# Kernel optimization log

Measured on AMD Instinct MI355X. Metric: run time of the kernel, lower is better.

Reference implementation:

```python
import jax, jax.numpy as jnp
import numpy as np

NUM_TOKENS = 16384
COMPACT = 8192
HIDDEN = 2048
INTER = 8192


def setup_inputs() -> dict:
    key = jax.random.key(0)
    k_x, k_fg, k_sc, k_wg, k_wu, k_wd = jax.random.split(key, 6)
    x = jax.random.normal(k_x, (NUM_TOKENS, HIDDEN), dtype=jnp.float32)
    fold_gather = jax.random.randint(k_fg, (COMPACT,), 0, NUM_TOKENS, dtype=jnp.int32)
    scatter_indices = jax.random.randint(k_sc, (NUM_TOKENS,), 0, COMPACT, dtype=jnp.int32)
    # torch nn.Linear weights are [out_features, in_features]
    s_h = 1.0 / np.sqrt(HIDDEN)
    s_i = 1.0 / np.sqrt(INTER)
    W_gate = jax.random.uniform(k_wg, (INTER, HIDDEN), jnp.float32, -s_h, s_h)
    W_up = jax.random.uniform(k_wu, (INTER, HIDDEN), jnp.float32, -s_h, s_h)
    W_down = jax.random.uniform(k_wd, (HIDDEN, INTER), jnp.float32, -s_i, s_i)
    return {"x": x, "W_gate": W_gate, "W_up": W_up, "W_down": W_down,
            "fold_gather": fold_gather, "scatter_indices": scatter_indices}


def reference(x, W_gate, W_up, W_down, fold_gather, scatter_indices):
    # gather original tokens into compact space
    x_compact = jnp.take(x, fold_gather, axis=0)               # [C, H]
    gate = jax.nn.silu(jnp.einsum('ch,ih->ci', x_compact, W_gate))  # [C, I]
    up = jnp.einsum('ch,ih->ci', x_compact, W_up)               # [C, I]
    down = jnp.einsum('ci,hi->ch', gate * up, W_down)           # [C, H]
    # scatter compact results back to every original token slot
    return jnp.take(down, scatter_indices, axis=0)              # [N, H]
```

## Files before the change

kernel.cpp:

```cpp
#include <hip/hip_runtime.h>
#include <hip/hip_bf16.h>
#include <stdint.h>

#define HIDDEN  2048
#define INTER   8192
#define COMPACT 8192
#define NTOK    16384

#define NT_GU (HIDDEN / 64)
#define NT_DN (INTER / 64)

typedef unsigned short ushort_t;
typedef float  f32x4  __attribute__((ext_vector_type(4)));
typedef __bf16 bf16x8 __attribute__((ext_vector_type(8)));

#define VMCNT(n) asm volatile("s_waitcnt vmcnt(" #n ")" ::: "memory")
#define FENCE()  asm volatile("" ::: "memory")
#define BARRIER() do { FENCE(); __builtin_amdgcn_s_barrier(); FENCE(); } while (0)

__device__ __align__(16) ushort_t g_xc[(size_t)COMPACT * HIDDEN];
__device__ __align__(16) ushort_t g_wg[(size_t)INTER * HIDDEN];
__device__ __align__(16) ushort_t g_wu[(size_t)INTER * HIDDEN];
__device__ __align__(16) ushort_t g_wd[(size_t)HIDDEN * INTER];
__device__ __align__(16) float    g_dn[(size_t)COMPACT * HIDDEN];

__device__ __forceinline__ ushort_t f2bf(float f) {
    uint32_t u = __builtin_bit_cast(uint32_t, f);
    uint32_t lsb = (u >> 16) & 1u;
    u += 0x7fffu + lsb;
    return (ushort_t)(u >> 16);
}

__device__ __forceinline__ void async_cp16(const void* g, void* l) {
    __builtin_amdgcn_global_load_lds(
        (__attribute__((address_space(1))) void*)((void*)g),
        (__attribute__((address_space(3))) void*)l,
        16, 0, 0);
}

__device__ __forceinline__ bf16x8 ldfrag(const ushort_t* m, int row, int slot) {
    return *(const bf16x8*)(m + row * 64 + slot * 8);
}

__global__ __launch_bounds__(256)
void k_gather_cast(const float* __restrict__ x, const int* __restrict__ fg)
{
    const int c = blockIdx.x;
    const int t = threadIdx.x;
    const float4* src = (const float4*)(x + (size_t)fg[c] * HIDDEN) + (t << 1);
    float4 a = src[0], b = src[1];
    union { ushort_t u[8]; uint4 v; } p;
    p.u[0] = f2bf(a.x); p.u[1] = f2bf(a.y); p.u[2] = f2bf(a.z); p.u[3] = f2bf(a.w);
    p.u[4] = f2bf(b.x); p.u[5] = f2bf(b.y); p.u[6] = f2bf(b.z); p.u[7] = f2bf(b.w);
    *((uint4*)(g_xc + (size_t)c * HIDDEN) + t) = p.v;
}

template<int W>
__global__ __launch_bounds__(256)
void k_cast(const float* __restrict__ src)
{
    ushort_t* __restrict__ dst = (W == 0) ? g_wg : (W == 1) ? g_wu : g_wd;
    const size_t g = (size_t)blockIdx.x * 256 + threadIdx.x;
    const float4* s = (const float4*)src + (g << 1);
    float4 a = s[0], b = s[1];
    union { ushort_t u[8]; uint4 v; } p;
    p.u[0] = f2bf(a.x); p.u[1] = f2bf(a.y); p.u[2] = f2bf(a.z); p.u[3] = f2bf(a.w);
    p.u[4] = f2bf(b.x); p.u[5] = f2bf(b.y); p.u[6] = f2bf(b.z); p.u[7] = f2bf(b.w);
    *((uint4*)dst + g) = p.v;
}

#define MFMA16(ACC, AF, BF)                                                    \
    _Pragma("unroll")                                                          \
    for (int i = 0; i < 4; ++i)                                                \
        _Pragma("unroll")                                                      \
        for (int j = 0; j < 2; ++j) {                                          \
            ACC[i][j] = __builtin_amdgcn_mfma_f32_16x16x32_bf16(AF[i][0], BF[j][0], ACC[i][j], 0, 0, 0); \
            ACC[i][j] = __builtin_amdgcn_mfma_f32_16x16x32_bf16(AF[i][1], BF[j][1], ACC[i][j], 0, 0, 0); \
        }

__global__ __launch_bounds__(512, 2)
void k_gateup(ushort_t* __restrict__ h)
{
    __shared__ __align__(16) ushort_t As[2][256 * 64];
    __shared__ __align__(16) ushort_t Gs[2][128 * 64];
    __shared__ __align__(16) ushort_t Us[2][128 * 64];

    const int tid  = threadIdx.x;
    const int lane = tid & 63;
    const int wv   = tid >> 6;
    const int wr   = wv >> 2;
    const int wc   = wv & 3;
    const int lr   = lane & 15;
    const int q    = lane >> 4;
    const int sl0  = q ^ (lr & 7);
    const int sl1  = sl0 ^ 4;
    const int srow = tid >> 3;
    const int scol = ((lane & 7) ^ (lane >> 3)) << 3;
    const int lofs = tid * 8;

    const int bm0 = blockIdx.y << 8;
    const int bn0 = blockIdx.x << 7;

    const ushort_t* pA = g_xc + (size_t)(bm0 + srow) * HIDDEN + scol;
    const ushort_t* pG = g_wg + (size_t)(bn0 + srow) * HIDDEN + scol;
    const ushort_t* pU = g_wu + (size_t)(bn0 + srow) * HIDDEN + scol;
    const size_t rS = (size_t)64 * HIDDEN;

    f32x4 ag0[4][2], ag1[4][2], au0[4][2], au1[4][2];
    #pragma unroll
    for (int i = 0; i < 4; ++i)
        #pragma unroll
        for (int j = 0; j < 2; ++j) {
            ag0[i][j] = (f32x4){0.f,0.f,0.f,0.f};
            ag1[i][j] = (f32x4){0.f,0.f,0.f,0.f};
            au0[i][j] = (f32x4){0.f,0.f,0.f,0.f};
            au1[i][j] = (f32x4){0.f,0.f,0.f,0.f};
        }

    {
        ushort_t* An = As[0]; ushort_t* Gn = Gs[0]; ushort_t* Un = Us[0];
        async_cp16(pA,          An + lofs);
        async_cp16(pA + rS,     An + 4096 + lofs);
        async_cp16(pG,          Gn + lofs);
        async_cp16(pG + rS,     Gn + 4096 + lofs);
        async_cp16(pU,          Un + lofs);
        async_cp16(pU + rS,     Un + 4096 + lofs);
        async_cp16(pA + 2*rS,   An + 8192 + lofs);
        async_cp16(pA + 3*rS,   An + 12288 + lofs);
        pA += 64; pG += 64; pU += 64;
        VMCNT(0);
        BARRIER();
    }

    for (int t = 0; t < NT_GU; ++t) {
        const ushort_t* Ac = As[t & 1];
        const ushort_t* Gc = Gs[t & 1];
        const ushort_t* Uc = Us[t & 1];
        ushort_t* An = As[(t & 1) ^ 1];
        ushort_t* Gn = Gs[(t & 1) ^ 1];
        ushort_t* Un = Us[(t & 1) ^ 1];
        const bool more = (t + 1 < NT_GU);

        bf16x8 af[4][2], bg[2][2], bu[2][2];

        #pragma unroll
        for (int i = 0; i < 4; ++i) {
            const int row = wr * 64 + i * 16 + lr;
            af[i][0] = ldfrag(Ac, row, sl0);
            af[i][1] = ldfrag(Ac, row, sl1);
        }
        #pragma unroll
        for (int j = 0; j < 2; ++j) {
            const int row = wc * 32 + j * 16 + lr;
            bg[j][0] = ldfrag(Gc, row, sl0);
            bg[j][1] = ldfrag(Gc, row, sl1);
        }
        if (more) {
            async_cp16(pA,      An + lofs);
            async_cp16(pA + rS, An + 4096 + lofs);
            VMCNT(4);
        } else {
            VMCNT(2);
        }
        BARRIER();
        __builtin_amdgcn_s_setprio(1);
        MFMA16(ag0, af, bg);
        __builtin_amdgcn_s_setprio(0);
        BARRIER();

        #pragma unroll
        for (int j = 0; j < 2; ++j) {
            const int row = wc * 32 + j * 16 + lr;
            bu[j][0] = ldfrag(Uc, row, sl0);
            bu[j][1] = ldfrag(Uc, row, sl1);
        }
        if (more) {
            async_cp16(pG,      Gn + lofs);
            async_cp16(pG + rS, Gn + 4096 + lofs);
            VMCNT(4);
        } else {
            VMCNT(0);
        }
        BARRIER();
        __builtin_amdgcn_s_setprio(1);
        MFMA16(au0, af, bu);
        __builtin_amdgcn_s_setprio(0);
        BARRIER();

        #pragma unroll
        for (int i = 0; i < 4; ++i) {
            const int row = 128 + wr * 64 + i * 16 + lr;
            af[i][0] = ldfrag(Ac, row, sl0);
            af[i][1] = ldfrag(Ac, row, sl1);
        }
        if (more) {
            async_cp16(pU,      Un + lofs);
            async_cp16(pU + rS, Un + 4096 + lofs);
        }
        BARRIER();
        __builtin_amdgcn_s_setprio(1);
        MFMA16(ag1, af, bg);
        __builtin_amdgcn_s_setprio(0);
        BARRIER();

        if (more) {
            async_cp16(pA + 2*rS, An + 8192 + lofs);
            async_cp16(pA + 3*rS, An + 12288 + lofs);
        }
        VMCNT(4);
        BARRIER();
        __builtin_amdgcn_s_setprio(1);
        MFMA16(au1, af, bu);
        __builtin_amdgcn_s_setprio(0);
        BARRIER();

        pA += 64; pG += 64; pU += 64;
    }

    const int or0 = bm0 + wr * 64 + (q << 2);
    const int oc  = bn0 + wc * 32 + lr;
    #define GU_STORE(AG, AU, MH)                                               \
        _Pragma("unroll")                                                      \
        for (int i = 0; i < 4; ++i)                                            \
            _Pragma("unroll")                                                  \
            for (int j = 0; j < 2; ++j)                                        \
                _Pragma("unroll")                                              \
                for (int r = 0; r < 4; ++r) {                                  \
                    float g = AG[i][j][r];                                     \
                    float u = AU[i][j][r];                                     \
                    float s = g / (1.0f + __expf(-g));                         \
                    h[(size_t)(or0 + (MH)*128 + i*16 + r) * INTER + (oc + j*16)] = f2bf(s * u); \
                }
    GU_STORE(ag0, au0, 0)
    GU_STORE(ag1, au1, 1)
    #undef GU_STORE
}

__global__ __launch_bounds__(512, 2)
void k_down(const ushort_t* __restrict__ hbuf)
{
    __shared__ __align__(16) ushort_t As[2][256 * 64];
    __shared__ __align__(16) ushort_t Bs[2][256 * 64];

    const int tid  = threadIdx.x;
    const int lane = tid & 63;
    const int wv   = tid >> 6;
    const int wr   = wv >> 2;
    const int wc   = wv & 3;
    const int lr   = lane & 15;
    const int q    = lane >> 4;
    const int sl0  = q ^ (lr & 7);
    const int sl1  = sl0 ^ 4;
    const int srow = tid >> 3;
    const int scol = ((lane & 7) ^ (lane >> 3)) << 3;
    const int lofs = tid * 8;

    const int bm0 = blockIdx.y << 8;
    const int bn0 = blockIdx.x << 8;

    const ushort_t* pH = hbuf + (size_t)(bm0 + srow) * INTER + scol;
    const ushort_t* pW = g_wd + (size_t)(bn0 + srow) * INTER + scol;
    const size_t rS = (size_t)64 * INTER;

    f32x4 c00[4][2], c01[4][2], c10[4][2], c11[4][2];
    #pragma unroll
    for (int i = 0; i < 4; ++i)
        #pragma unroll
        for (int j = 0; j < 2; ++j) {
            c00[i][j] = (f32x4){0.f,0.f,0.f,0.f};
            c01[i][j] = (f32x4){0.f,0.f,0.f,0.f};
            c10[i][j] = (f32x4){0.f,0.f,0.f,0.f};
            c11[i][j] = (f32x4){0.f,0.f,0.f,0.f};
        }

    {
        ushort_t* An = As[0]; ushort_t* Bn = Bs[0];
        async_cp16(pH,          An + lofs);
        async_cp16(pH + rS,     An + 4096 + lofs);
        async_cp16(pW,          Bn + lofs);
        async_cp16(pW + rS,     Bn + 4096 + lofs);
        async_cp16(pW + 2*rS,   Bn + 8192 + lofs);
        async_cp16(pW + 3*rS,   Bn + 12288 + lofs);
        async_cp16(pH + 2*rS,   An + 8192 + lofs);
        async_cp16(pH + 3*rS,   An + 12288 + lofs);
        pH += 64; pW += 64;
        VMCNT(0);
        BARRIER();
    }

    for (int t = 0; t < NT_DN; ++t) {
        const ushort_t* Ac = As[t & 1];
        const ushort_t* Bc = Bs[t & 1];
        ushort_t* An = As[(t & 1) ^ 1];
        ushort_t* Bn = Bs[(t & 1) ^ 1];
        const bool more = (t + 1 < NT_DN);

        bf16x8 af[4][2], b0[2][2], b1[2][2];

        #pragma unroll
        for (int i = 0; i < 4; ++i) {
            const int row = wr * 64 + i * 16 + lr;
            af[i][0] = ldfrag(Ac, row, sl0);
            af[i][1] = ldfrag(Ac, row, sl1);
        }
        #pragma unroll
        for (int j = 0; j < 2; ++j) {
            const int row = wc * 32 + j * 16 + lr;
            b0[j][0] = ldfrag(Bc, row, sl0);
            b0[j][1] = ldfrag(Bc, row, sl1);
        }
        if (more) {
            async_cp16(pH,      An + lofs);
            async_cp16(pH + rS, An + 4096 + lofs);
            VMCNT(4);
        } else {
            VMCNT(2);
        }
        BARRIER();
        __builtin_amdgcn_s_setprio(1);
        MFMA16(c00, af, b0);
        __builtin_amdgcn_s_setprio(0);
        BARRIER();

        #pragma unroll
        for (int j = 0; j < 2; ++j) {
            const int row = 128 + wc * 32 + j * 16 + lr;
            b1[j][0] = ldfrag(Bc, row, sl0);
            b1[j][1] = ldfrag(Bc, row, sl1);
        }
        if (more) {
            async_cp16(pW,      Bn + lofs);
            async_cp16(pW + rS, Bn + 4096 + lofs);
            VMCNT(4);
        } else {
            VMCNT(0);
        }
        BARRIER();
        __builtin_amdgcn_s_setprio(1);
        MFMA16(c01, af, b1);
        __builtin_amdgcn_s_setprio(0);
        BARRIER();

        #pragma unroll
        for (int i = 0; i < 4; ++i) {
            const int row = 128 + wr * 64 + i * 16 + lr;
            af[i][0] = ldfrag(Ac, row, sl0);
            af[i][1] = ldfrag(Ac, row, sl1);
        }
        if (more) {
            async_cp16(pW + 2*rS, Bn + 8192 + lofs);
            async_cp16(pW + 3*rS, Bn + 12288 + lofs);
        }
        BARRIER();
        __builtin_amdgcn_s_setprio(1);
        MFMA16(c10, af, b0);
        __builtin_amdgcn_s_setprio(0);
        BARRIER();

        if (more) {
            async_cp16(pH + 2*rS, An + 8192 + lofs);
            async_cp16(pH + 3*rS, An + 12288 + lofs);
        }
        VMCNT(4);
        BARRIER();
        __builtin_amdgcn_s_setprio(1);
        MFMA16(c11, af, b1);
        __builtin_amdgcn_s_setprio(0);
        BARRIER();

        pH += 64; pW += 64;
    }

    const int or0 = bm0 + wr * 64 + (q << 2);
    const int oc  = bn0 + wc * 32 + lr;
    #define DN_STORE(CC, MH, NH)                                               \
        _Pragma("unroll")                                                      \
        for (int i = 0; i < 4; ++i)                                            \
            _Pragma("unroll")                                                  \
            for (int j = 0; j < 2; ++j)                                        \
                _Pragma("unroll")                                              \
                for (int r = 0; r < 4; ++r)                                    \
                    g_dn[(size_t)(or0 + (MH)*128 + i*16 + r) * HIDDEN + (oc + (NH)*128 + j*16)] = CC[i][j][r];
    DN_STORE(c00, 0, 0)
    DN_STORE(c01, 0, 1)
    DN_STORE(c10, 1, 0)
    DN_STORE(c11, 1, 1)
    #undef DN_STORE
}

__global__ __launch_bounds__(256)
void k_scatter(const int* __restrict__ sc,
               float4* __restrict__ out)
{
    const int gid = blockIdx.x * 256 + threadIdx.x;
    const int row = gid >> 9;
    const int ch  = gid & 511;
    const int s = sc[row];
    out[((size_t)row << 9) + ch] = ((const float4*)g_dn)[((size_t)s << 9) + ch];
}

extern "C" void kernel_launch(void* const* d_in, const int* in_sizes, int n_in,
                              void* d_out, int out_size, void* d_ws, size_t ws_size,
                              hipStream_t stream)
{
    (void)in_sizes; (void)n_in; (void)out_size; (void)d_ws; (void)ws_size;

    const float* x  = (const float*)d_in[0];
    const float* Wg = (const float*)d_in[1];
    const float* Wu = (const float*)d_in[2];
    const float* Wd = (const float*)d_in[3];
    const int* fg = (const int*)d_in[4];
    const int* sc = (const int*)d_in[5];
    float* out = (float*)d_out;

    ushort_t* h = (ushort_t*)d_out;

    k_gather_cast<<<COMPACT, 256, 0, stream>>>(x, fg);
    k_cast<0><<<(INTER * HIDDEN / 8) / 256, 256, 0, stream>>>(Wg);
    k_cast<1><<<(INTER * HIDDEN / 8) / 256, 256, 0, stream>>>(Wu);
    k_cast<2><<<(HIDDEN * INTER / 8) / 256, 256, 0, stream>>>(Wd);

    k_gateup<<<dim3(INTER / 128, COMPACT / 256), 512, 0, stream>>>(h);
    k_down<<<dim3(HIDDEN / 256, COMPACT / 256), 512, 0, stream>>>(h);
    k_scatter<<<(NTOK * HIDDEN / 4) / 256, 256, 0, stream>>>(
        sc, (float4*)out);
}
```

Measured before the change: 1.377 ms.

## Issue all next-tile loads up front and remap blocks for XCD-local L2 reuse

```diff
diff --git a/kernel.cpp b/kernel.cpp
--- a/kernel.cpp
+++ b/kernel.cpp
@@ -15,8 +15,7 @@
 typedef __bf16 bf16x8 __attribute__((ext_vector_type(8)));
 
 #define VMCNT(n) asm volatile("s_waitcnt vmcnt(" #n ")" ::: "memory")
-#define FENCE()  asm volatile("" ::: "memory")
-#define BARRIER() do { FENCE(); __builtin_amdgcn_s_barrier(); FENCE(); } while (0)
+#define BARRIER() do { asm volatile("" ::: "memory"); __builtin_amdgcn_s_barrier(); asm volatile("" ::: "memory"); } while (0)
 
 __device__ __align__(16) ushort_t g_xc[(size_t)COMPACT * HIDDEN];
 __device__ __align__(16) ushort_t g_wg[(size_t)INTER * HIDDEN];
@@ -98,8 +97,11 @@
     const int scol = ((lane & 7) ^ (lane >> 3)) << 3;
     const int lofs = tid * 8;
 
-    const int bm0 = blockIdx.y << 8;
-    const int bn0 = blockIdx.x << 7;
+    const int orig = blockIdx.y * 64 + blockIdx.x;
+    const int xcd  = orig & 7;
+    const int jj   = orig >> 3;
+    const int bn0  = ((xcd << 3) | (jj & 7)) << 7;
+    const int bm0  = (jj >> 3) << 8;
 
     const ushort_t* pA = g_xc + (size_t)(bm0 + srow) * HIDDEN + scol;
     const ushort_t* pG = g_wg + (size_t)(bn0 + srow) * HIDDEN + scol;
@@ -128,7 +130,7 @@
         async_cp16(pA + 2*rS,   An + 8192 + lofs);
         async_cp16(pA + 3*rS,   An + 12288 + lofs);
         pA += 64; pG += 64; pU += 64;
-        VMCNT(0);
+        VMCNT(4);
         BARRIER();
     }
 
@@ -156,16 +158,20 @@
             bg[j][1] = ldfrag(Gc, row, sl1);
         }
         if (more) {
-            async_cp16(pA,      An + lofs);
-            async_cp16(pA + rS, An + 4096 + lofs);
-            VMCNT(4);
-        } else {
-            VMCNT(2);
+            async_cp16(pA,        An + lofs);
+            async_cp16(pA + rS,   An + 4096 + lofs);
+            async_cp16(pG,        Gn + lofs);
+            async_cp16(pG + rS,   Gn + 4096 + lofs);
+            async_cp16(pU,        Un + lofs);
+            async_cp16(pU + rS,   Un + 4096 + lofs);
+            async_cp16(pA + 2*rS, An + 8192 + lofs);
+            async_cp16(pA + 3*rS, An + 12288 + lofs);
         }
         BARRIER();
         __builtin_amdgcn_s_setprio(1);
         MFMA16(ag0, af, bg);
         __builtin_amdgcn_s_setprio(0);
+        if (more) { VMCNT(10); } else { VMCNT(2); }
         BARRIER();
 
         #pragma unroll
@@ -174,17 +180,11 @@
             bu[j][0] = ldfrag(Uc, row, sl0);
             bu[j][1] = ldfrag(Uc, row, sl1);
         }
-        if (more) {
-            async_cp16(pG,      Gn + lofs);
-            async_cp16(pG + rS, Gn + 4096 + lofs);
-            VMCNT(4);
-        } else {
-            VMCNT(0);
-        }
         BARRIER();
         __builtin_amdgcn_s_setprio(1);
         MFMA16(au0, af, bu);
         __builtin_amdgcn_s_setprio(0);
+        if (more) { VMCNT(8); } else { VMCNT(0); }
         BARRIER();
 
         #pragma unroll
@@ -193,25 +193,16 @@
             af[i][0] = ldfrag(Ac, row, sl0);
             af[i][1] = ldfrag(Ac, row, sl1);
         }
-        if (more) {
-            async_cp16(pU,      Un + lofs);
-            async_cp16(pU + rS, Un + 4096 + lofs);
-        }
         BARRIER();
         __builtin_amdgcn_s_setprio(1);
         MFMA16(ag1, af, bg);
         __builtin_amdgcn_s_setprio(0);
         BARRIER();
 
-        if (more) {
-            async_cp16(pA + 2*rS, An + 8192 + lofs);
-            async_cp16(pA + 3*rS, An + 12288 + lofs);
-        }
-        VMCNT(4);
-        BARRIER();
         __builtin_amdgcn_s_setprio(1);
         MFMA16(au1, af, bu);
         __builtin_amdgcn_s_setprio(0);
+        if (more) { VMCNT(4); }
         BARRIER();
 
         pA += 64; pG += 64; pU += 64;
@@ -255,8 +246,11 @@
     const int scol = ((lane & 7) ^ (lane >> 3)) << 3;
     const int lofs = tid * 8;
 
-    const int bm0 = blockIdx.y << 8;
-    const int bn0 = blockIdx.x << 8;
+    const int orig = blockIdx.y * 8 + blockIdx.x;
+    const int xcd  = orig & 7;
+    const int jj   = orig >> 3;
+    const int bn0  = (jj & 7) << 8;
+    const int bm0  = ((xcd << 2) | (jj >> 3)) << 8;
 
     const ushort_t* pH = hbuf + (size_t)(bm0 + srow) * INTER + scol;
     const ushort_t* pW = g_wd + (size_t)(bn0 + srow) * INTER + scol;
@@ -284,7 +278,7 @@
         async_cp16(pH + 2*rS,   An + 8192 + lofs);
         async_cp16(pH + 3*rS,   An + 12288 + lofs);
         pH += 64; pW += 64;
-        VMCNT(0);
+        VMCNT(4);
         BARRIER();
     }
 
@@ -310,16 +304,20 @@
             b0[j][1] = ldfrag(Bc, row, sl1);
         }
         if (more) {
-            async_cp16(pH,      An + lofs);
-            async_cp16(pH + rS, An + 4096 + lofs);
-            VMCNT(4);
-        } else {
-            VMCNT(2);
+            async_cp16(pH,        An + lofs);
+            async_cp16(pH + rS,   An + 4096 + lofs);
+            async_cp16(pW,        Bn + lofs);
+            async_cp16(pW + rS,   Bn + 4096 + lofs);
+            async_cp16(pW + 2*rS, Bn + 8192 + lofs);
+            async_cp16(pW + 3*rS, Bn + 12288 + lofs);
+            async_cp16(pH + 2*rS, An + 8192 + lofs);
+            async_cp16(pH + 3*rS, An + 12288 + lofs);
         }
         BARRIER();
         __builtin_amdgcn_s_setprio(1);
         MFMA16(c00, af, b0);
         __builtin_amdgcn_s_setprio(0);
+        if (more) { VMCNT(10); } else { VMCNT(2); }
         BARRIER();
 
         #pragma unroll
@@ -328,17 +326,11 @@
             b1[j][0] = ldfrag(Bc, row, sl0);
             b1[j][1] = ldfrag(Bc, row, sl1);
         }
-        if (more) {
-            async_cp16(pW,      Bn + lofs);
-            async_cp16(pW + rS, Bn + 4096 + lofs);
-            VMCNT(4);
-        } else {
-            VMCNT(0);
-        }
         BARRIER();
         __builtin_amdgcn_s_setprio(1);
         MFMA16(c01, af, b1);
         __builtin_amdgcn_s_setprio(0);
+        if (more) { VMCNT(8); } else { VMCNT(0); }
         BARRIER();
 
         #pragma unroll
@@ -347,25 +339,16 @@
             af[i][0] = ldfrag(Ac, row, sl0);
             af[i][1] = ldfrag(Ac, row, sl1);
         }
-        if (more) {
-            async_cp16(pW + 2*rS, Bn + 8192 + lofs);
-            async_cp16(pW + 3*rS, Bn + 12288 + lofs);
-        }
         BARRIER();
         __builtin_amdgcn_s_setprio(1);
         MFMA16(c10, af, b0);
         __builtin_amdgcn_s_setprio(0);
         BARRIER();
 
-        if (more) {
-            async_cp16(pH + 2*rS, An + 8192 + lofs);
-            async_cp16(pH + 3*rS, An + 12288 + lofs);
-        }
-        VMCNT(4);
-        BARRIER();
         __builtin_amdgcn_s_setprio(1);
         MFMA16(c11, af, b1);
         __builtin_amdgcn_s_setprio(0);
+        if (more) { VMCNT(4); }
         BARRIER();
 
         pH += 64; pW += 64;
```

Result: slower. 1.479 ms (+7.4%).
